# Performance work log

Measured on AMD Instinct MI355X. Metric: run time of the kernel, lower is better.

Reference implementation:

```python
import jax, jax.numpy as jnp
import numpy as np
from jax import lax

B, T, D_BERT, H_LSTM, L = 32, 512, 768, 256, 9


def setup_inputs() -> dict:
    key = jax.random.key(0)
    ks = jax.random.split(key, 10)
    def rn(k, shape, s=0.02):
        return jax.random.normal(k, shape, dtype=jnp.float32) * s
    return {
        "seq_out": jax.random.normal(ks[0], (B, T, D_BERT), dtype=jnp.float32),
        "attention_mask": jnp.ones((B, T), dtype=jnp.int32),
        "labels": jax.random.randint(ks[1], (B, T), 0, L),
        "w_ih_f": rn(ks[2], (4 * H_LSTM, D_BERT)),
        "w_hh_f": rn(ks[3], (4 * H_LSTM, H_LSTM)),
        "b_f": jnp.zeros((4 * H_LSTM,), jnp.float32),
        "w_ih_b": rn(ks[4], (4 * H_LSTM, D_BERT)),
        "w_hh_b": rn(ks[5], (4 * H_LSTM, H_LSTM)),
        "b_b": jnp.zeros((4 * H_LSTM,), jnp.float32),
        "w_tag": rn(ks[6], (L, 2 * H_LSTM)),
        "b_tag": jnp.zeros((L,), jnp.float32),
        "start_trans": rn(ks[7], (L,), 0.1),
        "end_trans": rn(ks[8], (L,), 0.1),
        "trans": rn(ks[9], (L, L), 0.1),
    }


def _lstm_dir(x, w_ih, w_hh, b):
    # x: [T, B, D]; torch gate order: i, f, g, o
    Bb, H = x.shape[1], w_hh.shape[1]
    def step(carry, x_t):
        h, c = carry
        g = x_t @ w_ih.T + h @ w_hh.T + b
        i, f, gg, o = jnp.split(g, 4, axis=-1)
        c = jax.nn.sigmoid(f) * c + jax.nn.sigmoid(i) * jnp.tanh(gg)
        h = jax.nn.sigmoid(o) * jnp.tanh(c)
        return (h, c), h
    init = (jnp.zeros((Bb, H), x.dtype), jnp.zeros((Bb, H), x.dtype))
    _, hs = lax.scan(step, init, x)
    return hs  # [T, B, H]


def _emissions(seq_out, w_ih_f, w_hh_f, b_f, w_ih_b, w_hh_b, b_b, w_tag, b_tag):
    x = seq_out.transpose(1, 0, 2)  # [T, B, D]
    hf = _lstm_dir(x, w_ih_f, w_hh_f, b_f)
    hb = _lstm_dir(x[::-1], w_ih_b, w_hh_b, b_b)[::-1]
    h = jnp.concatenate([hf, hb], axis=-1)  # [T, B, 2H] (dropout: eval mode, identity)
    return (h @ w_tag.T + b_tag).transpose(1, 0, 2).astype(jnp.float32)  # [B, T, L]


def _crf_llh(em, tags, mask, start, end, trans):
    # numerator: score of the gold path
    em_sc = jnp.take_along_axis(em, tags[..., None], axis=2)[..., 0]  # [B, T]
    tr_sc = trans[tags[:, :-1], tags[:, 1:]]  # [B, T-1]
    num = start[tags[:, 0]] + em_sc[:, 0] + jnp.sum((tr_sc + em_sc[:, 1:]) * mask[:, 1:], axis=1)
    last_idx = (jnp.sum(mask, axis=1) - 1).astype(jnp.int32)
    last_tags = jnp.take_along_axis(tags, last_idx[:, None], axis=1)[:, 0]
    num = num + end[last_tags]
    # denominator: log-partition via forward algorithm (sequential logsumexp scan)
    def step(score, inp):
        em_t, m_t = inp
        nxt = jax.nn.logsumexp(score[:, :, None] + trans[None] + em_t[:, None, :], axis=1)
        return jnp.where(m_t[:, None] > 0, nxt, score), None
    score0 = start + em[:, 0]
    score, _ = lax.scan(step, score0, (em[:, 1:].transpose(1, 0, 2), mask[:, 1:].T))
    denom = jax.nn.logsumexp(score + end, axis=1)
    return num - denom


def _crf_decode(em, mask, start, end, trans):
    Ll = em.shape[2]
    def step(score, inp):
        em_t, m_t = inp
        comb = score[:, :, None] + trans[None]  # [B, prev, cur]
        nxt = jnp.max(comb, axis=1) + em_t
        bp = jnp.argmax(comb, axis=1)  # [B, L]
        keep = m_t[:, None] > 0
        return jnp.where(keep, nxt, score), jnp.where(keep, bp, jnp.arange(Ll)[None, :])
    score0 = start + em[:, 0]
    final, bps = lax.scan(step, score0, (em[:, 1:].transpose(1, 0, 2), mask[:, 1:].T))
    last = jnp.argmax(final + end, axis=1)  # [B]
    def back(tag, bp_t):
        prev = jnp.take_along_axis(bp_t, tag[:, None], axis=1)[:, 0]
        return prev, prev
    _, earlier = lax.scan(back, last, bps, reverse=True)  # [T-1, B]
    return jnp.concatenate([earlier, last[None]], axis=0).T  # [B, T]


def reference(seq_out, attention_mask, labels, w_ih_f, w_hh_f, b_f, w_ih_b, w_hh_b, b_b, w_tag, b_tag, start_trans, end_trans, trans):
    em = _emissions(seq_out, w_ih_f, w_hh_f, b_f, w_ih_b, w_hh_b, b_b, w_tag, b_tag)
    mask = attention_mask.astype(jnp.float32)
    lbl = jnp.where(labels == -100, 0, labels)
    loss = -jnp.mean(_crf_llh(em, lbl, mask, start_trans, end_trans, trans))
    preds = _crf_decode(em, attention_mask, start_trans, end_trans, trans)
    return em, loss, preds
```

## Files before the change

kernel.cpp:

```cpp
#include <hip/hip_runtime.h>
#include <cmath>


#define NB 32
#define NT 512
#define ND 768
#define NH 256
#define NG 1024
#define NC 2048
#define NL 9
#define NHC 512

static const size_t OFF_WIHT  = 0;
static const size_t OFF_WHHT  = 1572864;
static const size_t OFF_XPART = OFF_WHHT + 524288;
static const size_t OFF_HCAT  = OFF_XPART + 33554432;

__global__ void prep(const float* __restrict__ wihf, const float* __restrict__ wihb,
                     const float* __restrict__ whhf, const float* __restrict__ whhb,
                     float* __restrict__ w_ihT, float* __restrict__ w_hhT,
                     float* __restrict__ d_loss) {
  int idx = blockIdx.x * 256 + threadIdx.x;
  if (idx == 0) d_loss[0] = 0.f;
  if (idx < 1572864) {
    int k = idx >> 11;
    int c = idx & 2047;
    int d = c >> 10;
    int j = c & 1023;
    w_ihT[idx] = d ? wihb[j * ND + k] : wihf[j * ND + k];
  } else {
    int i2 = idx - 1572864;
    int d = i2 >> 18;
    int r = i2 & 262143;
    int k = r >> 10;
    int j = r & 1023;
    w_hhT[i2] = d ? whhb[j * NH + k] : whhf[j * NH + k];
  }
}

__global__ __launch_bounds__(256, 2)
void gemm_x(const float* __restrict__ x, const float* __restrict__ wT,
            const float* __restrict__ bf, const float* __restrict__ bb,
            float* __restrict__ xpart) {
  __shared__ float As[8][128];
  __shared__ float Bs[8][128];
  const int tid = threadIdx.x;
  const int tx = tid & 15, ty = tid >> 4;
  const int r0 = blockIdx.y * 128, c0 = blockIdx.x * 128;

  float acc[8][8] = {};

  const int arow = tid >> 1;
  const int akq  = (tid & 1) * 4;
  const int rA = r0 + arow;
  const float* aptr = x + ((size_t)((rA & 31) * NT + (rA >> 5)) * ND) + akq;
  const int bk = tid >> 5;
  const int bc = (tid & 31) * 4;
  const float* bptr = wT + (size_t)bk * NC + c0 + bc;

  for (int k0 = 0; k0 < ND; k0 += 8) {
    float4 av = *(const float4*)(aptr + k0);
    float4 bv = *(const float4*)(bptr + (size_t)k0 * NC);
    __syncthreads();
    As[akq + 0][arow] = av.x;
    As[akq + 1][arow] = av.y;
    As[akq + 2][arow] = av.z;
    As[akq + 3][arow] = av.w;
    *(float4*)&Bs[bk][bc] = bv;
    __syncthreads();
#pragma unroll
    for (int k = 0; k < 8; ++k) {
      float4 a0 = *(const float4*)&As[k][ty * 8];
      float4 a1 = *(const float4*)&As[k][ty * 8 + 4];
      float4 b0 = *(const float4*)&Bs[k][tx * 8];
      float4 b1 = *(const float4*)&Bs[k][tx * 8 + 4];
      float am[8] = {a0.x, a0.y, a0.z, a0.w, a1.x, a1.y, a1.z, a1.w};
      float bm[8] = {b0.x, b0.y, b0.z, b0.w, b1.x, b1.y, b1.z, b1.w};
#pragma unroll
      for (int i = 0; i < 8; ++i)
#pragma unroll
        for (int j = 0; j < 8; ++j) acc[i][j] += am[i] * bm[j];
    }
  }

  const int cbase = c0 + tx * 8;
  float bias[8];
#pragma unroll
  for (int j = 0; j < 8; ++j) {
    int c = cbase + j;
    bias[j] = (c < NG) ? bf[c] : bb[c - NG];
  }
#pragma unroll
  for (int i = 0; i < 8; ++i) {
    int r = r0 + ty * 8 + i;
    float4 v0 = {acc[i][0] + bias[0], acc[i][1] + bias[1],
                 acc[i][2] + bias[2], acc[i][3] + bias[3]};
    float4 v1 = {acc[i][4] + bias[4], acc[i][5] + bias[5],
                 acc[i][6] + bias[6], acc[i][7] + bias[7]};
    *(float4*)(xpart + (size_t)r * NC + cbase) = v0;
    *(float4*)(xpart + (size_t)r * NC + cbase + 4) = v1;
  }
}

__global__ __launch_bounds__(256, 1)
void lstm_scan(const float* __restrict__ whhT, const float* __restrict__ xpart,
               float* __restrict__ hcat) {
  __shared__ float hS[NH];
  __shared__ float gS[NG];
  const int tid = threadIdx.x;
  const int d = blockIdx.x >> 5;
  const int b = blockIdx.x & 31;
  const float* wT = whhT + (size_t)d * (NH * NG);
  float c = 0.f;
  hS[tid] = 0.f;
  __syncthreads();
  const int j0 = tid * 4;
  for (int s = 0; s < NT; ++s) {
    const int t = d ? (NT - 1 - s) : s;
    const float* xp = xpart + ((size_t)(t * NB + b) * NC) + d * NG + j0;
    float4 acc = *(const float4*)xp;
#pragma unroll 8
    for (int k = 0; k < NH; ++k) {
      float hk = hS[k];
      float4 w = *(const float4*)(wT + (size_t)k * NG + j0);
      acc.x += hk * w.x;
      acc.y += hk * w.y;
      acc.z += hk * w.z;
      acc.w += hk * w.w;
    }
    *(float4*)&gS[j0] = acc;
    __syncthreads();
    float gi = gS[tid], gf = gS[NH + tid], gg = gS[2 * NH + tid], go = gS[3 * NH + tid];
    float ii = 1.f / (1.f + expf(-gi));
    float ff = 1.f / (1.f + expf(-gf));
    float tg = tanhf(gg);
    float oo = 1.f / (1.f + expf(-go));
    c = ff * c + ii * tg;
    float h = oo * tanhf(c);
    hS[tid] = h;
    hcat[((size_t)(b * NT + t)) * NHC + d * NH + tid] = h;
    __syncthreads();
  }
}

__global__ void emissions(const float* __restrict__ hcat, const float* __restrict__ wtag,
                          const float* __restrict__ btag, float* __restrict__ em) {
  __shared__ float wS[NL * NHC];
  const int tid = threadIdx.x;
  for (int i = tid; i < NL * NHC; i += 256) wS[i] = wtag[i];
  __syncthreads();
  const int w = tid >> 6, l = tid & 63;
  const int r = blockIdx.x * 4 + w;
  const float* hp = hcat + (size_t)r * NHC;
  float acc[NL] = {};
#pragma unroll
  for (int rep = 0; rep < 8; ++rep) {
    float hv = hp[l + rep * 64];
#pragma unroll
    for (int j = 0; j < NL; ++j) acc[j] += hv * wS[j * NHC + l + rep * 64];
  }
#pragma unroll
  for (int j = 0; j < NL; ++j) {
#pragma unroll
    for (int off = 32; off; off >>= 1) acc[j] += __shfl_xor(acc[j], off, 64);
  }
  if (l == 0) {
#pragma unroll
    for (int j = 0; j < NL; ++j) em[(size_t)r * NL + j] = acc[j] + btag[j];
  }
}

__global__ void crf_fwd(const float* __restrict__ em, const int* __restrict__ mask,
                        const int* __restrict__ labels, const float* __restrict__ start,
                        const float* __restrict__ endt, const float* __restrict__ trans,
                        float* __restrict__ d_loss) {
  __shared__ float emS[NT * NL];
  __shared__ float maskS[NT];
  __shared__ int lblS[NT];
  const int b = blockIdx.x;
  const int tid = threadIdx.x;
  for (int i = tid; i < NT * NL; i += 64) emS[i] = em[(size_t)b * NT * NL + i];
  for (int i = tid; i < NT; i += 64) {
    maskS[i] = (float)mask[b * NT + i];
    int lb = labels[b * NT + i];
    lblS[i] = (lb == -100) ? 0 : lb;
  }
  __syncthreads();

  float part = 0.f, msum = 0.f;
  for (int t = tid; t < NT; t += 64) {
    msum += maskS[t];
    if (t >= 1)
      part += (trans[lblS[t - 1] * NL + lblS[t]] + emS[t * NL + lblS[t]]) * maskS[t];
  }
#pragma unroll
  for (int off = 32; off; off >>= 1) {
    part += __shfl_xor(part, off, 64);
    msum += __shfl_xor(msum, off, 64);
  }

  const int j = tid >> 2, q = tid & 3;
  const bool leader = (q == 0) && (j < NL);
  float tr0 = 0.f, tr1 = 0.f, tr2 = -1e30f;
  float score = 0.f;
  if (tid < 36) {
    tr0 = trans[q * NL + j];
    tr1 = trans[(q + 4) * NL + j];
    if (q == 0) tr2 = trans[8 * NL + j];
    if (leader) score = start[j] + emS[j];
  }
  for (int t = 1; t < NT; ++t) {
    float s0 = __shfl(score, q * 4, 64);
    float s1 = __shfl(score, (q + 4) * 4, 64);
    float s2 = __shfl(score, 32, 64);
    float v0 = s0 + tr0, v1 = s1 + tr1;
    float v2 = (q == 0) ? (s2 + tr2) : -1e30f;
    float m = fmaxf(fmaxf(v0, v1), v2);
    m = fmaxf(m, __shfl_xor(m, 1, 4));
    m = fmaxf(m, __shfl_xor(m, 2, 4));
    float e = expf(v0 - m) + expf(v1 - m) + ((q == 0) ? expf(v2 - m) : 0.f);
    e += __shfl_xor(e, 1, 4);
    e += __shfl_xor(e, 2, 4);
    if (leader) {
      float nxt = m + logf(e) + emS[t * NL + j];
      score = (maskS[t] > 0.f) ? nxt : score;
    }
  }
  float vs[NL];
  float mx = -1e30f;
#pragma unroll
  for (int jj = 0; jj < NL; ++jj) {
    float sj = __shfl(score, jj * 4, 64) + endt[jj];
    vs[jj] = sj;
    mx = fmaxf(mx, sj);
  }
  float se = 0.f;
#pragma unroll
  for (int jj = 0; jj < NL; ++jj) se += expf(vs[jj] - mx);
  float denom = mx + logf(se);
  if (tid == 0) {
    int li = (int)(msum - 0.5f);
    float num = start[lblS[0]] + emS[lblS[0]] + part + endt[lblS[li]];
    atomicAdd(d_loss, -(num - denom) * (1.f / 32.f));
  }
}

__global__ void crf_viterbi(const float* __restrict__ em, const int* __restrict__ mask,
                            const float* __restrict__ start, const float* __restrict__ endt,
                            const float* __restrict__ trans, float* __restrict__ preds) {
  __shared__ float emS[NT * NL];
  __shared__ int maskS[NT];
  __shared__ short bpS[(NT - 1) * NL];
  __shared__ short tagS[NT];
  const int b = blockIdx.x;
  const int tid = threadIdx.x;
  for (int i = tid; i < NT * NL; i += 64) emS[i] = em[(size_t)b * NT * NL + i];
  for (int i = tid; i < NT; i += 64) maskS[i] = mask[b * NT + i];
  __syncthreads();

  const int j = tid >> 2, q = tid & 3;
  const bool leader = (q == 0) && (j < NL);
  float tr0 = 0.f, tr1 = 0.f, tr2 = -1e30f;
  float score = 0.f;
  if (tid < 36) {
    tr0 = trans[q * NL + j];
    tr1 = trans[(q + 4) * NL + j];
    if (q == 0) tr2 = trans[8 * NL + j];
    if (leader) score = start[j] + emS[j];
  }
  for (int t = 1; t < NT; ++t) {
    float s0 = __shfl(score, q * 4, 64);
    float s1 = __shfl(score, (q + 4) * 4, 64);
    float s2 = __shfl(score, 32, 64);
    float v0 = s0 + tr0, v1 = s1 + tr1;
    float v2 = (q == 0) ? (s2 + tr2) : -1e30f;
    float bv = v0;
    int bi = q;
    if (v1 > bv) { bv = v1; bi = q + 4; }
    if (q == 0 && v2 > bv) { bv = v2; bi = 8; }
#pragma unroll
    for (int off = 1; off <= 2; off <<= 1) {
      float ov = __shfl_xor(bv, off, 4);
      int oi = __shfl_xor(bi, off, 4);
      if (ov > bv || (ov == bv && oi < bi)) { bv = ov; bi = oi; }
    }
    if (leader) {
      int keep = maskS[t];
      float nxt = bv + emS[t * NL + j];
      bpS[(t - 1) * NL + j] = keep ? (short)bi : (short)j;
      score = keep ? nxt : score;
    }
  }
  float fv[NL];
#pragma unroll
  for (int jj = 0; jj < NL; ++jj) fv[jj] = __shfl(score, jj * 4, 64) + endt[jj];
  if (tid == 0) {
    int last = 0;
    float bvv = fv[0];
#pragma unroll
    for (int jj = 1; jj < NL; ++jj)
      if (fv[jj] > bvv) { bvv = fv[jj]; last = jj; }
    tagS[NT - 1] = (short)last;
    for (int t = NT - 1; t >= 1; --t) tagS[t - 1] = bpS[(t - 1) * NL + tagS[t]];
  }
  __syncthreads();
  for (int i = tid; i < NT; i += 64) preds[(size_t)b * NT + i] = (float)tagS[i];
}

extern "C" void kernel_launch(void* const* d_in, const int* in_sizes, int n_in,
                              void* d_out, int out_size, void* d_ws, size_t ws_size,
                              hipStream_t stream) {
  const float* seq_out = (const float*)d_in[0];
  const int* attn = (const int*)d_in[1];
  const int* labels = (const int*)d_in[2];
  const float* w_ih_f = (const float*)d_in[3];
  const float* w_hh_f = (const float*)d_in[4];
  const float* b_f = (const float*)d_in[5];
  const float* w_ih_b = (const float*)d_in[6];
  const float* w_hh_b = (const float*)d_in[7];
  const float* b_b = (const float*)d_in[8];
  const float* w_tag = (const float*)d_in[9];
  const float* b_tag = (const float*)d_in[10];
  const float* start_t = (const float*)d_in[11];
  const float* end_t = (const float*)d_in[12];
  const float* trans = (const float*)d_in[13];
  (void)in_sizes; (void)n_in; (void)out_size; (void)ws_size;

  float* ws = (float*)d_ws;
  float* w_ihT = ws + OFF_WIHT;
  float* w_hhT = ws + OFF_WHHT;
  float* xpart = ws + OFF_XPART;
  float* hcat = ws + OFF_HCAT;

  float* em = (float*)d_out;
  float* d_loss = em + NB * NT * NL;
  float* preds = d_loss + 1;

  prep<<<8192, 256, 0, stream>>>(w_ih_f, w_ih_b, w_hh_f, w_hh_b, w_ihT, w_hhT, d_loss);
  gemm_x<<<dim3(16, 128), 256, 0, stream>>>(seq_out, w_ihT, b_f, b_b, xpart);
  lstm_scan<<<64, 256, 0, stream>>>(w_hhT, xpart, hcat);
  emissions<<<4096, 256, 0, stream>>>(hcat, w_tag, b_tag, em);
  crf_fwd<<<32, 64, 0, stream>>>(em, attn, labels, start_t, end_t, trans, d_loss);
  crf_viterbi<<<32, 64, 0, stream>>>(em, attn, start_t, end_t, trans, preds);
}
```

Before: 5.229 ms.

## Split LSTM recurrence across blocks by hidden units with weight-stationary LDS and grid sync

The LSTM scan previously gave each block one batch row and streamed the full recurrent weight matrix from global memory every timestep. Now each of 32 blocks per direction owns 8 hidden units (32 gate columns) for all 32 batch rows and keeps its weight slice resident in LDS. Hidden states are exchanged every step through a double-buffered global buffer, using per-step atomic counters and spin-waits as a cross-block barrier. This removes repeated weight reads from global memory and L2, but adds a grid-wide synchronisation per step and relies on all 64 blocks being co-resident. A timeout in the spin loop could silently produce wrong results if the blocks fall out of step.

```diff
diff --git a/kernel.cpp b/kernel.cpp
--- a/kernel.cpp
+++ b/kernel.cpp
@@ -10,18 +10,24 @@
 #define NC 2048
 #define NL 9
 #define NHC 512
+#define PPD 32
+#define HPAD 260
+#define NBUF (2 * NB * NH)
 
 static const size_t OFF_WIHT  = 0;
 static const size_t OFF_WHHT  = 1572864;
-static const size_t OFF_XPART = OFF_WHHT + 524288;
-static const size_t OFF_HCAT  = OFF_XPART + 33554432;
+static const size_t OFF_XPART = 2097152;
+static const size_t OFF_HCAT  = 35651584;
+static const size_t OFF_HG    = 44040192;
+static const size_t OFF_CTR   = 44072960;
 
 __global__ void prep(const float* __restrict__ wihf, const float* __restrict__ wihb,
                      const float* __restrict__ whhf, const float* __restrict__ whhb,
                      float* __restrict__ w_ihT, float* __restrict__ w_hhT,
-                     float* __restrict__ d_loss) {
+                     float* __restrict__ d_loss, int* __restrict__ ctr) {
   int idx = blockIdx.x * 256 + threadIdx.x;
   if (idx == 0) d_loss[0] = 0.f;
+  if (idx < 1024) ctr[idx] = 0;
   if (idx < 1572864) {
     int k = idx >> 11;
     int c = idx & 2047;
@@ -104,42 +110,99 @@
 
 __global__ __launch_bounds__(256, 1)
 void lstm_scan(const float* __restrict__ whhT, const float* __restrict__ xpart,
-               float* __restrict__ hcat) {
-  __shared__ float hS[NH];
-  __shared__ float gS[NG];
+               float* __restrict__ hcat, float* __restrict__ hG,
+               int* __restrict__ ctr) {
+  __shared__ float wS[256 * 32];
+  __shared__ float hS[32 * HPAD];
+  __shared__ float gS[32 * 36];
   const int tid = threadIdx.x;
   const int d = blockIdx.x >> 5;
-  const int b = blockIdx.x & 31;
-  const float* wT = whhT + (size_t)d * (NH * NG);
+  const int m = blockIdx.x & 31;
+
+  const float* wsrc = whhT + (size_t)d * NH * NG;
+  for (int it = 0; it < 32; ++it) {
+    int i = it * 256 + tid;
+    int k = i >> 5, l = i & 31;
+    int g = l >> 3, u2 = l & 7;
+    wS[k * 32 + l] = wsrc[(size_t)k * NG + g * 256 + m * 8 + u2];
+  }
+  for (int i = tid; i < 32 * HPAD; i += 256) hS[i] = 0.f;
+  __syncthreads();
+
+  const int b = tid >> 3;
+  const int cg = tid & 7;
+  const int u = tid & 7;
+  const int l0 = cg * 4;
+  const int g4 = l0 >> 3, u04 = l0 & 7;
+  const int col4 = g4 * 256 + m * 8 + u04;
+  int* ctrd = ctr + d * NT;
+
   float c = 0.f;
-  hS[tid] = 0.f;
-  __syncthreads();
-  const int j0 = tid * 4;
   for (int s = 0; s < NT; ++s) {
     const int t = d ? (NT - 1 - s) : s;
-    const float* xp = xpart + ((size_t)(t * NB + b) * NC) + d * NG + j0;
-    float4 acc = *(const float4*)xp;
-#pragma unroll 8
-    for (int k = 0; k < NH; ++k) {
-      float hk = hS[k];
-      float4 w = *(const float4*)(wT + (size_t)k * NG + j0);
-      acc.x += hk * w.x;
-      acc.y += hk * w.y;
-      acc.z += hk * w.z;
-      acc.w += hk * w.w;
-    }
-    *(float4*)&gS[j0] = acc;
+    float4 xv = *(const float4*)(xpart + ((size_t)(t * NB + b) * NC) + d * NG + col4);
+    float4 acc = {0.f, 0.f, 0.f, 0.f};
+    const float* hrow = &hS[b * HPAD];
+    for (int k0 = 0; k0 < NH; k0 += 4) {
+      float4 hv = *(const float4*)(hrow + k0);
+      {
+        float4 wv = *(const float4*)(&wS[(k0 + 0) * 32 + l0]);
+        acc.x += hv.x * wv.x; acc.y += hv.x * wv.y; acc.z += hv.x * wv.z; acc.w += hv.x * wv.w;
+      }
+      {
+        float4 wv = *(const float4*)(&wS[(k0 + 1) * 32 + l0]);
+        acc.x += hv.y * wv.x; acc.y += hv.y * wv.y; acc.z += hv.y * wv.z; acc.w += hv.y * wv.w;
+      }
+      {
+        float4 wv = *(const float4*)(&wS[(k0 + 2) * 32 + l0]);
+        acc.x += hv.z * wv.x; acc.y += hv.z * wv.y; acc.z += hv.z * wv.z; acc.w += hv.z * wv.w;
+      }
+      {
+        float4 wv = *(const float4*)(&wS[(k0 + 3) * 32 + l0]);
+        acc.x += hv.w * wv.x; acc.y += hv.w * wv.y; acc.z += hv.w * wv.z; acc.w += hv.w * wv.w;
+      }
+    }
+    acc.x += xv.x; acc.y += xv.y; acc.z += xv.z; acc.w += xv.w;
+    *(float4*)(&gS[b * 36 + l0]) = acc;
     __syncthreads();
-    float gi = gS[tid], gf = gS[NH + tid], gg = gS[2 * NH + tid], go = gS[3 * NH + tid];
+
+    float gi = gS[b * 36 + u];
+    float gf = gS[b * 36 + 8 + u];
+    float gg = gS[b * 36 + 16 + u];
+    float go = gS[b * 36 + 24 + u];
     float ii = 1.f / (1.f + expf(-gi));
     float ff = 1.f / (1.f + expf(-gf));
     float tg = tanhf(gg);
     float oo = 1.f / (1.f + expf(-go));
     c = ff * c + ii * tg;
     float h = oo * tanhf(c);
-    hS[tid] = h;
-    hcat[((size_t)(b * NT + t)) * NHC + d * NH + tid] = h;
-    __syncthreads();
+    hcat[((size_t)(b * NT + t)) * NHC + d * NH + m * 8 + u] = h;
+
+    if (s < NT - 1) {
+      float* buf = hG + ((s & 1) ? NBUF : 0) + d * (NB * NH);
+      buf[b * NH + m * 8 + u] = h;
+      __threadfence();
+      __syncthreads();
+      if (tid == 0)
+        __hip_atomic_fetch_add(&ctrd[s], 1, __ATOMIC_RELEASE,
+                               __HIP_MEMORY_SCOPE_AGENT);
+      if ((tid & 63) == 0) {
+        long long t0 = wall_clock64();
+        while (__hip_atomic_load(&ctrd[s], __ATOMIC_ACQUIRE,
+                                 __HIP_MEMORY_SCOPE_AGENT) < PPD) {
+          __builtin_amdgcn_s_sleep(1);
+          if (wall_clock64() - t0 > 5000000LL) break;
+        }
+      }
+      __syncthreads();
+      __threadfence();
+      for (int i = tid; i < 2048; i += 256) {
+        float4 v = *(const float4*)(buf + i * 4);
+        int bb = i >> 6, kk = (i & 63) * 4;
+        *(float4*)(&hS[bb * HPAD + kk]) = v;
+      }
+      __syncthreads();
+    }
   }
 }
 
@@ -331,14 +394,16 @@
   float* w_hhT = ws + OFF_WHHT;
   float* xpart = ws + OFF_XPART;
   float* hcat = ws + OFF_HCAT;
+  float* hG = ws + OFF_HG;
+  int* ctr = (int*)(ws + OFF_CTR);
 
   float* em = (float*)d_out;
   float* d_loss = em + NB * NT * NL;
   float* preds = d_loss + 1;
 
-  prep<<<8192, 256, 0, stream>>>(w_ih_f, w_ih_b, w_hh_f, w_hh_b, w_ihT, w_hhT, d_loss);
+  prep<<<8192, 256, 0, stream>>>(w_ih_f, w_ih_b, w_hh_f, w_hh_b, w_ihT, w_hhT, d_loss, ctr);
   gemm_x<<<dim3(16, 128), 256, 0, stream>>>(seq_out, w_ihT, b_f, b_b, xpart);
-  lstm_scan<<<64, 256, 0, stream>>>(w_hhT, xpart, hcat);
+  lstm_scan<<<64, 256, 0, stream>>>(w_hhT, xpart, hcat, hG, ctr);
   emissions<<<4096, 256, 0, stream>>>(hcat, w_tag, b_tag, em);
   crf_fwd<<<32, 64, 0, stream>>>(em, attn, labels, start_t, end_t, trans, d_loss);
   crf_viterbi<<<32, 64, 0, stream>>>(em, attn, start_t, end_t, trans, preds);
```

New measurement: 11.67 ms. 123% more time.
